# Optimization experiments

Measured on AMD Instinct MI355X. Metric: run time of the kernel, lower is better.

Reference implementation:

```python
import jax, jax.numpy as jnp
import numpy as np

B, N, D, H = 4, 4096, 128, 4
LN_EPS = 1e-5
SIG_EPS = 1e-6


def setup_inputs() -> dict:
    key = jax.random.key(0)
    k1, k2 = jax.random.split(key)
    x = jax.random.normal(k1, (B, N, D), dtype=jnp.float32)
    log_sigmas = jnp.zeros((H, 1, 1), dtype=jnp.float32)
    proj_w = jax.random.normal(k2, (D, D), dtype=jnp.float32) * (1.0 / np.sqrt(D))
    proj_b = jnp.zeros((D,), dtype=jnp.float32)
    ln_gamma = jnp.ones((D,), dtype=jnp.float32)
    ln_beta = jnp.zeros((D,), dtype=jnp.float32)
    return {"x": x, "log_sigmas": log_sigmas, "proj_w": proj_w,
            "proj_b": proj_b, "ln_gamma": ln_gamma, "ln_beta": ln_beta}


def reference(x, log_sigmas, proj_w, proj_b, ln_gamma, ln_beta):
    # x: [b, n, d]
    # squared pairwise Euclidean distances: [b, n, n]
    x2 = jnp.sum(x * x, axis=-1)
    gram = jnp.einsum('bnd,bmd->bnm', x, x)
    dist_sq = jnp.maximum(x2[:, :, None] + x2[:, None, :] - 2.0 * gram, 0.0)
    # per-head RBF adjacency, averaged over heads: [b, n, n]
    sigmas = jnp.exp(log_sigmas).reshape(-1)  # [h]
    denom = 2.0 * sigmas ** 2 + SIG_EPS       # [h]
    adjs = jnp.exp(-dist_sq[:, None, :, :] / denom[None, :, None, None])  # [b,h,n,n]
    adj_final = adjs.mean(axis=1)              # [b, n, n]
    # diffusion + projection
    out = jnp.einsum('bnm,bmd->bnd', adj_final, x)
    out = out @ proj_w.T + proj_b
    # ELU + residual + LayerNorm
    y = jax.nn.elu(out) + x
    mu = jnp.mean(y, axis=-1, keepdims=True)
    var = jnp.mean((y - mu) ** 2, axis=-1, keepdims=True)
    return (y - mu) / jnp.sqrt(var + LN_EPS) * ln_gamma + ln_beta
```

## Files before the change

kernel.cpp:

```cpp
#include <hip/hip_runtime.h>
#include <hip/hip_bf16.h>

#define BB 4
#define NN 4096
#define DD 128

typedef __attribute__((ext_vector_type(8))) short bf16x8;
typedef __attribute__((ext_vector_type(16))) float f32x16;

__device__ __forceinline__ unsigned short f2bf(float f) {
    unsigned int u = __float_as_uint(f);
    return (unsigned short)((u + 0x7FFFu + ((u >> 16) & 1u)) >> 16);
}
__device__ __forceinline__ float bf2f(unsigned short s) {
    return __uint_as_float(((unsigned int)s) << 16);
}


__global__ __launch_bounds__(256) void prep_kernel(const float* __restrict__ x,
        short* __restrict__ xbF, short* __restrict__ vF, float* __restrict__ x2) {
    __shared__ short Ls[64 * 136];
    int tid = threadIdx.x;
    int r = tid >> 2, cq = tid & 3;
    size_t rowg = (size_t)blockIdx.x * 64 + r;
    const float* xp = x + rowg * DD + cq * 32;
    short tmp[32];
    float s = 0.f;
    #pragma unroll
    for (int i = 0; i < 8; ++i) {
        float4 v = ((const float4*)xp)[i];
        unsigned short b0 = f2bf(v.x), b1 = f2bf(v.y), b2 = f2bf(v.z), b3 = f2bf(v.w);
        tmp[i*4+0] = (short)b0; tmp[i*4+1] = (short)b1;
        tmp[i*4+2] = (short)b2; tmp[i*4+3] = (short)b3;
        float f0 = bf2f(b0), f1 = bf2f(b1), f2 = bf2f(b2), f3 = bf2f(b3);
        s += f0*f0 + f1*f1 + f2*f2 + f3*f3;
    }
    #pragma unroll
    for (int c = 0; c < 4; ++c) {
        uint4 v = ((uint4*)tmp)[c];
        *(uint4*)(xbF + (rowg >> 5) * 4096 + (size_t)(cq * 4 + c) * 256 + (rowg & 31) * 8) = v;
        *(uint4*)(&Ls[r * 136 + cq * 32 + c * 8]) = v;
    }
    s += __shfl_xor(s, 1); s += __shfl_xor(s, 2);
    if ((tid & 3) == 0) x2[rowg] = s;
    __syncthreads();
    int d = (tid & 63) + ((tid >> 7) << 6);
    int nh = (tid >> 6) & 1;
    short arr[32];
    #pragma unroll
    for (int i = 0; i < 32; ++i) arr[i] = Ls[(nh * 32 + i) * 136 + d];
    int blk = blockIdx.x;
    int b = blk >> 6;
    int mbase = (blk & 63) * 64 + nh * 32;
    size_t base = (size_t)b * 524288 + (size_t)(d >> 5) * 131072 + (size_t)(d & 31) * 8;
    #pragma unroll
    for (int c = 0; c < 4; ++c)
        *(uint4*)(vF + base + (size_t)((mbase >> 3) + c) * 256) = ((uint4*)arr)[c];
}

__global__ __launch_bounds__(256) void wt_kernel(const float* __restrict__ W,
                                                 short* __restrict__ wbF) {
    int t = blockIdx.x * 256 + threadIdx.x;
    int j = t >> 5, cq = t & 31;
    float4 v = *(const float4*)(W + j * 128 + cq * 4);
    uint2 pk;
    pk.x = (unsigned)f2bf(v.x) | ((unsigned)f2bf(v.y) << 16);
    pk.y = (unsigned)f2bf(v.z) | ((unsigned)f2bf(v.w) << 16);
    *(uint2*)(wbF + (j >> 5) * 4096 + (cq >> 1) * 256 + (j & 31) * 8 + (cq & 1) * 4) = pk;
}

__global__ __launch_bounds__(512, 2) void attn_kernel(
        const short* __restrict__ xbF, const short* __restrict__ vF,
        const float* __restrict__ x2, const short* __restrict__ wbF,
        const float* __restrict__ log_sigmas, const float* __restrict__ pb,
        const float* __restrict__ x, const float* __restrict__ gamma,
        const float* __restrict__ beta, float* __restrict__ out) {
    __shared__ char smem[50304] __attribute__((aligned(128)));
    short* Ws = (short*)smem;
    int* flags = (int*)(smem + 50176);

    int tid = threadIdx.x, lane = tid & 63, w = tid >> 6;
    int l5 = lane & 31, hi = lane >> 5;

    int bid = (blockIdx.x & 7) * 32 + (blockIdx.x >> 3);
    int b = bid >> 6, n0 = (bid & 63) * 64;

    const short* xf_b = xbF + (size_t)b * 524288;
    const short* vf_b = vF + (size_t)b * 524288;
    const float* x2b = x2 + (size_t)b * NN;

    float invd[4];
    #pragma unroll
    for (int h = 0; h < 4; ++h) {
        float sg = __expf(log_sigmas[h]);
        invd[h] = 1.0f / (2.0f * sg * sg + 1e-6f);
    }
    bool same = (invd[0] == invd[1]) && (invd[1] == invd[2]) && (invd[2] == invd[3]);
    float c0 = -invd[0];
    float invd_min = fminf(fminf(invd[0], invd[1]), fminf(invd[2], invd[3]));
    float thr = 30.0f / invd_min;

    bf16x8 qa[8], qb[8];
    {
        const short* qp = xf_b + (n0 >> 5) * 4096;
        #pragma unroll
        for (int ck = 0; ck < 8; ++ck) {
            qa[ck] = *(const bf16x8*)(qp + (2 * ck + hi) * 256 + l5 * 8);
            qb[ck] = *(const bf16x8*)(qp + 4096 + (2 * ck + hi) * 256 + l5 * 8);
        }
    }
    float x2nA = x2b[n0 + l5], x2nB = x2b[n0 + 32 + l5];

    f32x16 O;
    #pragma unroll
    for (int i = 0; i < 16; ++i) O[i] = 0.f;

    int fb = 0;
    for (int t = 0; t < NN / 256; ++t) {
        int m1 = t * 256;
        const short* kp = xf_b + (t * 8 + w) * 4096;
        bf16x8 kf[8];
        #pragma unroll
        for (int ck = 0; ck < 8; ++ck)
            kf[ck] = *(const bf16x8*)(kp + (2 * ck + hi) * 256 + l5 * 8);
        f32x16 SA, SB;
        #pragma unroll
        for (int i = 0; i < 16; ++i) { SA[i] = 0.f; SB[i] = 0.f; }
        #pragma unroll
        for (int ck = 0; ck < 8; ++ck) {
            SA = __builtin_amdgcn_mfma_f32_32x32x16_bf16(kf[ck], qa[ck], SA, 0, 0, 0);
            SB = __builtin_amdgcn_mfma_f32_32x32x16_bf16(kf[ck], qb[ck], SB, 0, 0, 0);
        }
        float4 xm[4];
        #pragma unroll
        for (int q = 0; q < 4; ++q)
            xm[q] = *(const float4*)(x2b + m1 + w * 32 + 8 * q + 4 * hi);
        float dv[32];
        #pragma unroll
        for (int q = 0; q < 4; ++q)
            #pragma unroll
            for (int r = 0; r < 4; ++r) {
                float m2 = ((const float*)&xm[q])[r];
                dv[q * 4 + r]      = x2nA + m2 - 2.0f * SA[q * 4 + r];
                dv[16 + q * 4 + r] = x2nB + m2 - 2.0f * SB[q * 4 + r];
            }
        float pmin = dv[0];
        #pragma unroll
        for (int i = 1; i < 32; ++i) pmin = fminf(pmin, dv[i]);
        bool skipw = __all(pmin > thr);

        if (skipw) {
            uint2 z; z.x = 0; z.y = 0;
            #pragma unroll
            for (int q = 0; q < 4; ++q) {
                *(uint2*)((char*)Ws + l5 * 512 + ((4 * w + q) ^ l5) * 16 + 8 * hi) = z;
                *(uint2*)((char*)Ws + (32 + l5) * 512 + ((4 * w + q) ^ l5) * 16 + 8 * hi) = z;
            }
        } else {
            #pragma unroll
            for (int h2 = 0; h2 < 2; ++h2) {
                int rowb = h2 * 32 + l5;
                #pragma unroll
                for (int q = 0; q < 4; ++q) {
                    float wv[4];
                    #pragma unroll
                    for (int r = 0; r < 4; ++r) {
                        float c = fmaxf(dv[h2 * 16 + q * 4 + r], 0.0f);
                        if (same) wv[r] = __expf(c * c0);
                        else wv[r] = 0.25f * (__expf(-c * invd[0]) + __expf(-c * invd[1]) +
                                              __expf(-c * invd[2]) + __expf(-c * invd[3]));
                    }
                    uint2 pk;
                    pk.x = (unsigned)f2bf(wv[0]) | ((unsigned)f2bf(wv[1]) << 16);
                    pk.y = (unsigned)f2bf(wv[2]) | ((unsigned)f2bf(wv[3]) << 16);
                    *(uint2*)((char*)Ws + rowb * 512 + ((4 * w + q) ^ l5) * 16 + 8 * hi) = pk;
                }
            }
        }
        if (lane == 0) flags[fb * 8 + w] = skipw ? 1 : 0;
        __syncthreads();
        const int4* fp = (const int4*)(flags + fb * 8);
        int4 f0 = fp[0], f1 = fp[1];
        bool allskip = (f0.x & f0.y & f0.z & f0.w & f1.x & f1.y & f1.z & f1.w) != 0;
        fb ^= 1;
        if (!allskip) {
            int db = w & 3, nh = w >> 2;
            const short* vp = vf_b + db * 131072 + (m1 >> 3) * 256;
            const char* wsr = (const char*)Ws + (nh * 32 + l5) * 512;
            #pragma unroll
            for (int ck = 0; ck < 16; ++ck) {
                bf16x8 af = *(const bf16x8*)(vp + (2 * ck + hi) * 256 + l5 * 8);
                bf16x8 bf = *(const bf16x8*)(wsr + (((2 * ck + hi) ^ l5) * 16));
                O = __builtin_amdgcn_mfma_f32_32x32x16_bf16(af, bf, O, 0, 0, 0);
            }
            __syncthreads();
        }
    }

    short* Obf = (short*)smem;
    {
        int db = w & 3, nh = w >> 2;
        int orow = nh * 32 + l5;
        #pragma unroll
        for (int q = 0; q < 4; ++q) {
            uint2 pk;
            pk.x = (unsigned)f2bf(O[q * 4 + 0]) | ((unsigned)f2bf(O[q * 4 + 1]) << 16);
            pk.y = (unsigned)f2bf(O[q * 4 + 2]) | ((unsigned)f2bf(O[q * 4 + 3]) << 16);
            *(uint2*)((char*)Obf + orow * 256 + ((4 * db + q) ^ (l5 & 15)) * 16 + 8 * hi) = pk;
        }
    }
    __syncthreads();

    float* Plds = (float*)(smem + 16384);
    {
        int jq = w & 3, nh2 = w >> 2;
        f32x16 P;
        #pragma unroll
        for (int i = 0; i < 16; ++i) P[i] = 0.f;
        const short* wp = wbF + jq * 4096;
        const char* obr = (const char*)Obf + (nh2 * 32 + l5) * 256;
        #pragma unroll
        for (int ck = 0; ck < 8; ++ck) {
            bf16x8 af = *(const bf16x8*)(obr + ((2 * ck + hi) ^ (l5 & 15)) * 16);
            bf16x8 bf = *(const bf16x8*)(wp + (2 * ck + hi) * 256 + l5 * 8);
            P = __builtin_amdgcn_mfma_f32_32x32x16_bf16(af, bf, P, 0, 0, 0);
        }
        float pbj = pb[jq * 32 + l5];
        #pragma unroll
        for (int q = 0; q < 4; ++q)
            #pragma unroll
            for (int r = 0; r < 4; ++r) {
                int prow = nh2 * 32 + 8 * q + 4 * hi + r;
                Plds[prow * 132 + jq * 32 + l5] = P[q * 4 + r] + pbj;
            }
    }
    __syncthreads();

    {
        int row = tid >> 3, part = tid & 7;
        const float* xr = x + ((size_t)b * NN + n0 + row) * DD + part * 16;
        float y[16];
        float sum = 0.f, ss = 0.f;
        #pragma unroll
        for (int c = 0; c < 4; ++c) {
            float4 pv = *(const float4*)(Plds + row * 132 + part * 16 + c * 4);
            float4 xv = *(const float4*)(xr + c * 4);
            #pragma unroll
            for (int k = 0; k < 4; ++k) {
                float p = ((const float*)&pv)[k];
                float e = (p > 0.f ? p : __expf(p) - 1.f) + ((const float*)&xv)[k];
                y[c * 4 + k] = e;
                sum += e; ss += e * e;
            }
        }
        sum += __shfl_xor(sum, 1); ss += __shfl_xor(ss, 1);
        sum += __shfl_xor(sum, 2); ss += __shfl_xor(ss, 2);
        sum += __shfl_xor(sum, 4); ss += __shfl_xor(ss, 4);
        float mu = sum * 0.0078125f;
        float var = fmaxf(ss * 0.0078125f - mu * mu, 0.f);
        float inv = rsqrtf(var + 1e-5f);
        float* op = out + ((size_t)b * NN + n0 + row) * DD + part * 16;
        #pragma unroll
        for (int c = 0; c < 4; ++c) {
            float4 gv = *(const float4*)(gamma + part * 16 + c * 4);
            float4 bv = *(const float4*)(beta + part * 16 + c * 4);
            float4 o;
            ((float*)&o)[0] = (y[c*4+0] - mu) * inv * ((const float*)&gv)[0] + ((const float*)&bv)[0];
            ((float*)&o)[1] = (y[c*4+1] - mu) * inv * ((const float*)&gv)[1] + ((const float*)&bv)[1];
            ((float*)&o)[2] = (y[c*4+2] - mu) * inv * ((const float*)&gv)[2] + ((const float*)&bv)[2];
            ((float*)&o)[3] = (y[c*4+3] - mu) * inv * ((const float*)&gv)[3] + ((const float*)&bv)[3];
            *(float4*)(op + c * 4) = o;
        }
    }
}

extern "C" void kernel_launch(void* const* d_in, const int* in_sizes, int n_in,
                              void* d_out, int out_size, void* d_ws, size_t ws_size,
                              hipStream_t stream) {
    const float* x  = (const float*)d_in[0];
    const float* ls = (const float*)d_in[1];
    const float* pw = (const float*)d_in[2];
    const float* pb = (const float*)d_in[3];
    const float* g  = (const float*)d_in[4];
    const float* be = (const float*)d_in[5];
    float* out = (float*)d_out;

    char* ws = (char*)d_ws;
    short* xbF = (short*)ws;
    short* vF  = (short*)(ws + (size_t)4 * 1024 * 1024);
    float* x2  = (float*)(ws + (size_t)8 * 1024 * 1024);
    short* wbF = (short*)(ws + (size_t)8 * 1024 * 1024 + 65536);

    prep_kernel<<<dim3(BB * NN / 64), dim3(256), 0, stream>>>(x, xbF, vF, x2);
    wt_kernel<<<dim3(16), dim3(256), 0, stream>>>(pw, wbF);
    attn_kernel<<<dim3(BB * NN / 64), dim3(512), 0, stream>>>(
        xbF, vF, x2, wbF, ls, pb, x, g, be, out);
}
```

Baseline: 50.67 us.

## Make waves process key tiles independently with LDS atomic accumulation, fuse prep kernels

The attention loop drops the per-tile block barriers and shared weight staging. Each wave now strides over its own 32-key tiles, converts its RBF weights into MFMA operand layout with cross-lane shuffles, multiplies them by V, and accumulates partial outputs into an fp32 LDS buffer using atomicAdd. Each wave also prefetches its next key tile. The weight-transpose kernel is merged into the prep kernel as extra blocks, which removes one launch. The aim is to remove barrier stalls and let waves skip far-away tiles independently, but the many LDS float atomics per tile could cost more than the barriers did.

```diff
diff --git a/kernel.cpp b/kernel.cpp
--- a/kernel.cpp
+++ b/kernel.cpp
@@ -9,25 +9,37 @@
 typedef __attribute__((ext_vector_type(16))) float f32x16;
 
 __device__ __forceinline__ unsigned short f2bf(float f) {
-    unsigned int u = __float_as_uint(f);
+    unsigned u = __float_as_uint(f);
     return (unsigned short)((u + 0x7FFFu + ((u >> 16) & 1u)) >> 16);
 }
 __device__ __forceinline__ float bf2f(unsigned short s) {
-    return __uint_as_float(((unsigned int)s) << 16);
-}
-
-
-__global__ __launch_bounds__(256) void prep_kernel(const float* __restrict__ x,
-        short* __restrict__ xbF, short* __restrict__ vF, float* __restrict__ x2) {
+    return __uint_as_float((unsigned)s << 16);
+}
+__device__ __forceinline__ unsigned pk2(float a, float b) {
+    return (unsigned)f2bf(a) | ((unsigned)f2bf(b) << 16);
+}
+
+
+__global__ __launch_bounds__(512) void prep_kernel(const float* __restrict__ x,
+        const float* __restrict__ W, short* __restrict__ xbF,
+        short* __restrict__ vF, short* __restrict__ wbF, float* __restrict__ x2) {
+    if (blockIdx.x >= 256) {
+        int t = (blockIdx.x - 256) * 512 + threadIdx.x;
+        int j = t >> 5, cq = t & 31;
+        float4 v = *(const float4*)(W + j * 128 + cq * 4);
+        uint2 pk; pk.x = pk2(v.x, v.y); pk.y = pk2(v.z, v.w);
+        *(uint2*)(wbF + (j >> 5) * 4096 + (cq >> 1) * 256 + (j & 31) * 8 + (cq & 1) * 4) = pk;
+        return;
+    }
     __shared__ short Ls[64 * 136];
     int tid = threadIdx.x;
-    int r = tid >> 2, cq = tid & 3;
+    int r = tid >> 3, cq = tid & 7;
     size_t rowg = (size_t)blockIdx.x * 64 + r;
-    const float* xp = x + rowg * DD + cq * 32;
-    short tmp[32];
+    const float* xp = x + rowg * DD + cq * 16;
+    short tmp[16];
     float s = 0.f;
     #pragma unroll
-    for (int i = 0; i < 8; ++i) {
+    for (int i = 0; i < 4; ++i) {
         float4 v = ((const float4*)xp)[i];
         unsigned short b0 = f2bf(v.x), b1 = f2bf(v.y), b2 = f2bf(v.z), b3 = f2bf(v.w);
         tmp[i*4+0] = (short)b0; tmp[i*4+1] = (short)b1;
@@ -36,37 +48,23 @@
         s += f0*f0 + f1*f1 + f2*f2 + f3*f3;
     }
     #pragma unroll
-    for (int c = 0; c < 4; ++c) {
+    for (int c = 0; c < 2; ++c) {
         uint4 v = ((uint4*)tmp)[c];
-        *(uint4*)(xbF + (rowg >> 5) * 4096 + (size_t)(cq * 4 + c) * 256 + (rowg & 31) * 8) = v;
-        *(uint4*)(&Ls[r * 136 + cq * 32 + c * 8]) = v;
-    }
-    s += __shfl_xor(s, 1); s += __shfl_xor(s, 2);
-    if ((tid & 3) == 0) x2[rowg] = s;
-    __syncthreads();
-    int d = (tid & 63) + ((tid >> 7) << 6);
-    int nh = (tid >> 6) & 1;
-    short arr[32];
-    #pragma unroll
-    for (int i = 0; i < 32; ++i) arr[i] = Ls[(nh * 32 + i) * 136 + d];
-    int blk = blockIdx.x;
-    int b = blk >> 6;
-    int mbase = (blk & 63) * 64 + nh * 32;
+        *(uint4*)(xbF + (rowg >> 5) * 4096 + (size_t)(cq * 2 + c) * 256 + (rowg & 31) * 8) = v;
+        *(uint4*)(&Ls[r * 136 + cq * 16 + c * 8]) = v;
+    }
+    s += __shfl_xor(s, 1); s += __shfl_xor(s, 2); s += __shfl_xor(s, 4);
+    if (cq == 0) x2[rowg] = s;
+    __syncthreads();
+    int d = tid & 127, q = tid >> 7;
+    short arr[16];
+    #pragma unroll
+    for (int i = 0; i < 16; ++i) arr[i] = Ls[(q * 16 + i) * 136 + d];
+    int blk = blockIdx.x, b = blk >> 6;
+    int g0 = (blk & 63) * 8 + q * 2;
     size_t base = (size_t)b * 524288 + (size_t)(d >> 5) * 131072 + (size_t)(d & 31) * 8;
-    #pragma unroll
-    for (int c = 0; c < 4; ++c)
-        *(uint4*)(vF + base + (size_t)((mbase >> 3) + c) * 256) = ((uint4*)arr)[c];
-}
-
-__global__ __launch_bounds__(256) void wt_kernel(const float* __restrict__ W,
-                                                 short* __restrict__ wbF) {
-    int t = blockIdx.x * 256 + threadIdx.x;
-    int j = t >> 5, cq = t & 31;
-    float4 v = *(const float4*)(W + j * 128 + cq * 4);
-    uint2 pk;
-    pk.x = (unsigned)f2bf(v.x) | ((unsigned)f2bf(v.y) << 16);
-    pk.y = (unsigned)f2bf(v.z) | ((unsigned)f2bf(v.w) << 16);
-    *(uint2*)(wbF + (j >> 5) * 4096 + (cq >> 1) * 256 + (j & 31) * 8 + (cq & 1) * 4) = pk;
+    *(uint4*)(vF + base + (size_t)g0 * 256)       = ((uint4*)arr)[0];
+    *(uint4*)(vF + base + (size_t)(g0 + 1) * 256) = ((uint4*)arr)[1];
 }
 
 __global__ __launch_bounds__(512, 2) void attn_kernel(
@@ -75,9 +73,8 @@
         const float* __restrict__ log_sigmas, const float* __restrict__ pb,
         const float* __restrict__ x, const float* __restrict__ gamma,
         const float* __restrict__ beta, float* __restrict__ out) {
-    __shared__ char smem[50304] __attribute__((aligned(128)));
-    short* Ws = (short*)smem;
-    int* flags = (int*)(smem + 50176);
+    __shared__ char smem[34816] __attribute__((aligned(128)));
+    float* O_lds = (float*)smem;
 
     int tid = threadIdx.x, lane = tid & 63, w = tid >> 6;
     int l5 = lane & 31, hi = lane >> 5;
@@ -88,6 +85,9 @@
     const short* xf_b = xbF + (size_t)b * 524288;
     const short* vf_b = vF + (size_t)b * 524288;
     const float* x2b = x2 + (size_t)b * NN;
+
+    #pragma unroll
+    for (int i = 0; i < 17; ++i) O_lds[tid + 512 * i] = 0.f;
 
     float invd[4];
     #pragma unroll
@@ -102,7 +102,7 @@
 
     bf16x8 qa[8], qb[8];
     {
-        const short* qp = xf_b + (n0 >> 5) * 4096;
+        const short* qp = xf_b + (size_t)(n0 >> 5) * 4096;
         #pragma unroll
         for (int ck = 0; ck < 8; ++ck) {
             qa[ck] = *(const bf16x8*)(qp + (2 * ck + hi) * 256 + l5 * 8);
@@ -111,128 +111,161 @@
     }
     float x2nA = x2b[n0 + l5], x2nB = x2b[n0 + 32 + l5];
 
-    f32x16 O;
-    #pragma unroll
-    for (int i = 0; i < 16; ++i) O[i] = 0.f;
-
-    int fb = 0;
-    for (int t = 0; t < NN / 256; ++t) {
-        int m1 = t * 256;
-        const short* kp = xf_b + (t * 8 + w) * 4096;
-        bf16x8 kf[8];
+    __syncthreads();
+
+    bf16x8 kc[8];
+    {
+        const short* kp = xf_b + (size_t)w * 4096;
         #pragma unroll
         for (int ck = 0; ck < 8; ++ck)
-            kf[ck] = *(const bf16x8*)(kp + (2 * ck + hi) * 256 + l5 * 8);
+            kc[ck] = *(const bf16x8*)(kp + (2 * ck + hi) * 256 + l5 * 8);
+    }
+
+    for (int s = w; s < 128; s += 8) {
+        bf16x8 kn[8];
+        if (s + 8 < 128) {
+            const short* kp = xf_b + (size_t)(s + 8) * 4096;
+            #pragma unroll
+            for (int ck = 0; ck < 8; ++ck)
+                kn[ck] = *(const bf16x8*)(kp + (2 * ck + hi) * 256 + l5 * 8);
+        }
+        float4 t0 = *(const float4*)(x2b + s * 32 + 4 * hi);
+        float4 t1 = *(const float4*)(x2b + s * 32 + 8 + 4 * hi);
+        float4 t2 = *(const float4*)(x2b + s * 32 + 16 + 4 * hi);
+        float4 t3 = *(const float4*)(x2b + s * 32 + 24 + 4 * hi);
+        float xmv[16];
+        xmv[0]=t0.x; xmv[1]=t0.y; xmv[2]=t0.z; xmv[3]=t0.w;
+        xmv[4]=t1.x; xmv[5]=t1.y; xmv[6]=t1.z; xmv[7]=t1.w;
+        xmv[8]=t2.x; xmv[9]=t2.y; xmv[10]=t2.z; xmv[11]=t2.w;
+        xmv[12]=t3.x; xmv[13]=t3.y; xmv[14]=t3.z; xmv[15]=t3.w;
+
         f32x16 SA, SB;
         #pragma unroll
         for (int i = 0; i < 16; ++i) { SA[i] = 0.f; SB[i] = 0.f; }
         #pragma unroll
         for (int ck = 0; ck < 8; ++ck) {
-            SA = __builtin_amdgcn_mfma_f32_32x32x16_bf16(kf[ck], qa[ck], SA, 0, 0, 0);
-            SB = __builtin_amdgcn_mfma_f32_32x32x16_bf16(kf[ck], qb[ck], SB, 0, 0, 0);
-        }
-        float4 xm[4];
-        #pragma unroll
-        for (int q = 0; q < 4; ++q)
-            xm[q] = *(const float4*)(x2b + m1 + w * 32 + 8 * q + 4 * hi);
-        float dv[32];
-        #pragma unroll
-        for (int q = 0; q < 4; ++q)
-            #pragma unroll
-            for (int r = 0; r < 4; ++r) {
-                float m2 = ((const float*)&xm[q])[r];
-                dv[q * 4 + r]      = x2nA + m2 - 2.0f * SA[q * 4 + r];
-                dv[16 + q * 4 + r] = x2nB + m2 - 2.0f * SB[q * 4 + r];
-            }
-        float pmin = dv[0];
-        #pragma unroll
-        for (int i = 1; i < 32; ++i) pmin = fminf(pmin, dv[i]);
-        bool skipw = __all(pmin > thr);
-
-        if (skipw) {
-            uint2 z; z.x = 0; z.y = 0;
-            #pragma unroll
-            for (int q = 0; q < 4; ++q) {
-                *(uint2*)((char*)Ws + l5 * 512 + ((4 * w + q) ^ l5) * 16 + 8 * hi) = z;
-                *(uint2*)((char*)Ws + (32 + l5) * 512 + ((4 * w + q) ^ l5) * 16 + 8 * hi) = z;
-            }
-        } else {
-            #pragma unroll
-            for (int h2 = 0; h2 < 2; ++h2) {
-                int rowb = h2 * 32 + l5;
+            SA = __builtin_amdgcn_mfma_f32_32x32x16_bf16(kc[ck], qa[ck], SA, 0, 0, 0);
+            SB = __builtin_amdgcn_mfma_f32_32x32x16_bf16(kc[ck], qb[ck], SB, 0, 0, 0);
+        }
+        float dvA[16], dvB[16];
+        #pragma unroll
+        for (int i = 0; i < 16; ++i) {
+            dvA[i] = x2nA + xmv[i] - 2.0f * SA[i];
+            dvB[i] = x2nB + xmv[i] - 2.0f * SB[i];
+        }
+        float pmin = dvA[0];
+        #pragma unroll
+        for (int i = 1; i < 16; ++i) pmin = fminf(pmin, dvA[i]);
+        #pragma unroll
+        for (int i = 0; i < 16; ++i) pmin = fminf(pmin, dvB[i]);
+
+        if (!__all(pmin > thr)) {
+            float wA[16], wB[16];
+            #pragma unroll
+            for (int i = 0; i < 16; ++i) {
+                float cA = fmaxf(dvA[i], 0.f), cB = fmaxf(dvB[i], 0.f);
+                if (same) {
+                    wA[i] = __expf(cA * c0);
+                    wB[i] = __expf(cB * c0);
+                } else {
+                    wA[i] = 0.25f * (__expf(-cA * invd[0]) + __expf(-cA * invd[1]) +
+                                     __expf(-cA * invd[2]) + __expf(-cA * invd[3]));
+                    wB[i] = 0.25f * (__expf(-cB * invd[0]) + __expf(-cB * invd[1]) +
+                                     __expf(-cB * invd[2]) + __expf(-cB * invd[3]));
+                }
+            }
+            unsigned pAlo[4], pAhi[4], pBlo[4], pBhi[4];
+            #pragma unroll
+            for (int G = 0; G < 4; ++G) {
+                pAlo[G] = pk2(wA[4*G+0], wA[4*G+1]);
+                pAhi[G] = pk2(wA[4*G+2], wA[4*G+3]);
+                pBlo[G] = pk2(wB[4*G+0], wB[4*G+1]);
+                pBhi[G] = pk2(wB[4*G+2], wB[4*G+3]);
+            }
+            uint4 fA[2], fB[2];
+            #pragma unroll
+            for (int ks = 0; ks < 2; ++ks) {
+                unsigned oAl = hi ? pAlo[2*ks+1] : pAlo[2*ks];
+                unsigned oAh = hi ? pAhi[2*ks+1] : pAhi[2*ks];
+                unsigned sAl = hi ? pAlo[2*ks]   : pAlo[2*ks+1];
+                unsigned sAh = hi ? pAhi[2*ks]   : pAhi[2*ks+1];
+                unsigned rAl = __shfl_xor(sAl, 32);
+                unsigned rAh = __shfl_xor(sAh, 32);
+                fA[ks].x = hi ? rAl : oAl;  fA[ks].y = hi ? rAh : oAh;
+                fA[ks].z = hi ? oAl : rAl;  fA[ks].w = hi ? oAh : rAh;
+                unsigned oBl = hi ? pBlo[2*ks+1] : pBlo[2*ks];
+                unsigned oBh = hi ? pBhi[2*ks+1] : pBhi[2*ks];
+                unsigned sBl = hi ? pBlo[2*ks]   : pBlo[2*ks+1];
+                unsigned sBh = hi ? pBhi[2*ks]   : pBhi[2*ks+1];
+                unsigned rBl = __shfl_xor(sBl, 32);
+                unsigned rBh = __shfl_xor(sBh, 32);
+                fB[ks].x = hi ? rBl : oBl;  fB[ks].y = hi ? rBh : oBh;
+                fB[ks].z = hi ? oBl : rBl;  fB[ks].w = hi ? oBh : rBh;
+            }
+            bf16x8 wfA0 = *(bf16x8*)&fA[0], wfA1 = *(bf16x8*)&fA[1];
+            bf16x8 wfB0 = *(bf16x8*)&fB[0], wfB1 = *(bf16x8*)&fB[1];
+            #pragma unroll
+            for (int db = 0; db < 4; ++db) {
+                const short* vp = vf_b + db * 131072 + (size_t)s * 4 * 256;
+                bf16x8 v0 = *(const bf16x8*)(vp + (size_t)(0 + hi) * 256 + l5 * 8);
+                bf16x8 v1 = *(const bf16x8*)(vp + (size_t)(2 + hi) * 256 + l5 * 8);
+                f32x16 DA, DB;
                 #pragma unroll
-                for (int q = 0; q < 4; ++q) {
-                    float wv[4];
-                    #pragma unroll
-                    for (int r = 0; r < 4; ++r) {
-                        float c = fmaxf(dv[h2 * 16 + q * 4 + r], 0.0f);
-                        if (same) wv[r] = __expf(c * c0);
-                        else wv[r] = 0.25f * (__expf(-c * invd[0]) + __expf(-c * invd[1]) +
-                                              __expf(-c * invd[2]) + __expf(-c * invd[3]));
-                    }
-                    uint2 pk;
-                    pk.x = (unsigned)f2bf(wv[0]) | ((unsigned)f2bf(wv[1]) << 16);
-                    pk.y = (unsigned)f2bf(wv[2]) | ((unsigned)f2bf(wv[3]) << 16);
-                    *(uint2*)((char*)Ws + rowb * 512 + ((4 * w + q) ^ l5) * 16 + 8 * hi) = pk;
+                for (int i = 0; i < 16; ++i) { DA[i] = 0.f; DB[i] = 0.f; }
+                DA = __builtin_amdgcn_mfma_f32_32x32x16_bf16(v0, wfA0, DA, 0, 0, 0);
+                DA = __builtin_amdgcn_mfma_f32_32x32x16_bf16(v1, wfA1, DA, 0, 0, 0);
+                DB = __builtin_amdgcn_mfma_f32_32x32x16_bf16(v0, wfB0, DB, 0, 0, 0);
+                DB = __builtin_amdgcn_mfma_f32_32x32x16_bf16(v1, wfB1, DB, 0, 0, 0);
+                #pragma unroll
+                for (int i = 0; i < 16; ++i) {
+                    int droff = (i & 3) + 8 * (i >> 2) + 4 * hi;
+                    atomicAdd(&O_lds[(db * 32 + droff) * 68 + l5], DA[i]);
+                    atomicAdd(&O_lds[(db * 32 + droff) * 68 + 32 + l5], DB[i]);
                 }
             }
         }
-        if (lane == 0) flags[fb * 8 + w] = skipw ? 1 : 0;
-        __syncthreads();
-        const int4* fp = (const int4*)(flags + fb * 8);
-        int4 f0 = fp[0], f1 = fp[1];
-        bool allskip = (f0.x & f0.y & f0.z & f0.w & f1.x & f1.y & f1.z & f1.w) != 0;
-        fb ^= 1;
-        if (!allskip) {
-            int db = w & 3, nh = w >> 2;
-            const short* vp = vf_b + db * 131072 + (m1 >> 3) * 256;
-            const char* wsr = (const char*)Ws + (nh * 32 + l5) * 512;
-            #pragma unroll
-            for (int ck = 0; ck < 16; ++ck) {
-                bf16x8 af = *(const bf16x8*)(vp + (2 * ck + hi) * 256 + l5 * 8);
-                bf16x8 bf = *(const bf16x8*)(wsr + (((2 * ck + hi) ^ l5) * 16));
-                O = __builtin_amdgcn_mfma_f32_32x32x16_bf16(af, bf, O, 0, 0, 0);
-            }
-            __syncthreads();
-        }
-    }
-
-    short* Obf = (short*)smem;
+        if (s + 8 < 128) {
+            #pragma unroll
+            for (int ck = 0; ck < 8; ++ck) kc[ck] = kn[ck];
+        }
+    }
+
+    __syncthreads();
+
+    int jq = w & 3, nh2 = w >> 2;
+    bf16x8 af[8];
+    #pragma unroll
+    for (int ck = 0; ck < 8; ++ck) {
+        unsigned u0, u1, u2, u3;
+        {
+            int dbase = ck * 16 + hi * 8;
+            int nn = nh2 * 32 + l5;
+            u0 = pk2(O_lds[(dbase + 0) * 68 + nn], O_lds[(dbase + 1) * 68 + nn]);
+            u1 = pk2(O_lds[(dbase + 2) * 68 + nn], O_lds[(dbase + 3) * 68 + nn]);
+            u2 = pk2(O_lds[(dbase + 4) * 68 + nn], O_lds[(dbase + 5) * 68 + nn]);
+            u3 = pk2(O_lds[(dbase + 6) * 68 + nn], O_lds[(dbase + 7) * 68 + nn]);
+        }
+        uint4 uu; uu.x = u0; uu.y = u1; uu.z = u2; uu.w = u3;
+        af[ck] = *(bf16x8*)&uu;
+    }
+    f32x16 P;
+    #pragma unroll
+    for (int i = 0; i < 16; ++i) P[i] = 0.f;
     {
-        int db = w & 3, nh = w >> 2;
-        int orow = nh * 32 + l5;
-        #pragma unroll
-        for (int q = 0; q < 4; ++q) {
-            uint2 pk;
-            pk.x = (unsigned)f2bf(O[q * 4 + 0]) | ((unsigned)f2bf(O[q * 4 + 1]) << 16);
-            pk.y = (unsigned)f2bf(O[q * 4 + 2]) | ((unsigned)f2bf(O[q * 4 + 3]) << 16);
-            *(uint2*)((char*)Obf + orow * 256 + ((4 * db + q) ^ (l5 & 15)) * 16 + 8 * hi) = pk;
-        }
-    }
-    __syncthreads();
-
-    float* Plds = (float*)(smem + 16384);
-    {
-        int jq = w & 3, nh2 = w >> 2;
-        f32x16 P;
-        #pragma unroll
-        for (int i = 0; i < 16; ++i) P[i] = 0.f;
         const short* wp = wbF + jq * 4096;
-        const char* obr = (const char*)Obf + (nh2 * 32 + l5) * 256;
         #pragma unroll
         for (int ck = 0; ck < 8; ++ck) {
-            bf16x8 af = *(const bf16x8*)(obr + ((2 * ck + hi) ^ (l5 & 15)) * 16);
             bf16x8 bf = *(const bf16x8*)(wp + (2 * ck + hi) * 256 + l5 * 8);
-            P = __builtin_amdgcn_mfma_f32_32x32x16_bf16(af, bf, P, 0, 0, 0);
-        }
-        float pbj = pb[jq * 32 + l5];
-        #pragma unroll
-        for (int q = 0; q < 4; ++q)
-            #pragma unroll
-            for (int r = 0; r < 4; ++r) {
-                int prow = nh2 * 32 + 8 * q + 4 * hi + r;
-                Plds[prow * 132 + jq * 32 + l5] = P[q * 4 + r] + pbj;
-            }
+            P = __builtin_amdgcn_mfma_f32_32x32x16_bf16(af[ck], bf, P, 0, 0, 0);
+        }
+    }
+    float pbj = pb[jq * 32 + l5];
+    __syncthreads();
+    float* Plds = (float*)smem;
+    #pragma unroll
+    for (int i = 0; i < 16; ++i) {
+        int roff = (i & 3) + 8 * (i >> 2) + 4 * hi;
+        Plds[(nh2 * 32 + roff) * 132 + jq * 32 + l5] = P[i] + pbj;
     }
     __syncthreads();
 
@@ -291,8 +324,7 @@
     float* x2  = (float*)(ws + (size_t)8 * 1024 * 1024);
     short* wbF = (short*)(ws + (size_t)8 * 1024 * 1024 + 65536);
 
-    prep_kernel<<<dim3(BB * NN / 64), dim3(256), 0, stream>>>(x, xbF, vF, x2);
-    wt_kernel<<<dim3(16), dim3(256), 0, stream>>>(pw, wbF);
+    prep_kernel<<<dim3(264), dim3(512), 0, stream>>>(x, pw, xbF, vF, wbF, x2);
     attn_kernel<<<dim3(BB * NN / 64), dim3(512), 0, stream>>>(
         xbF, vF, x2, wbF, ls, pb, x, g, be, out);
 }
```

Result: slower. 57.87 us (+14.2%).
